# Kernel tuning notes

Measured on AMD Instinct MI355X. Metric: run time of the kernel, lower is better.

Reference implementation:

```python
import jax, jax.numpy as jnp
import numpy as np

N_NODES = 50000


def setup_inputs() -> dict:
    key = jax.random.key(0)
    k1, k2, k3, k4 = jax.random.split(key, 4)
    in_dim, out_dim, n_edges = 128, 64, 800000
    x = jax.random.normal(k1, (N_NODES, in_dim), dtype=jnp.float32)
    edge_index = jax.random.randint(k2, (2, n_edges), 0, N_NODES, dtype=jnp.int64)
    W = jax.random.normal(k3, (in_dim, out_dim), dtype=jnp.float32) * (1.0 / np.sqrt(in_dim))
    att = jax.random.normal(k4, (2 * out_dim,), dtype=jnp.float32) * (1.0 / np.sqrt(2 * out_dim))
    return {"x": x, "edge_index": edge_index, "W": W, "att": att}


def reference(x, edge_index, W, att):
    N = x.shape[0]
    F_out = W.shape[1]
    h = x @ W                                   # [N, F]
    src, dst = edge_index[0], edge_index[1]
    hs = h[src]                                 # [E, F] gather
    hd = h[dst]                                 # [E, F] gather
    # att(cat([h_src, h_dst])) == h_src @ a1 + h_dst @ a2
    a1, a2 = att[:F_out], att[F_out:]
    logit = jax.nn.leaky_relu(hs @ a1 + hd @ a2, 0.2)   # [E]
    E = logit.shape[0]
    # The original builds a dense [N, E] matrix (row d holds logit_e at col e
    # for dst[e]==d, zeros elsewhere) and softmaxes over the E axis. The
    # equivalent sparse form: denom_d = sum_{e:dst=d} exp(logit_e) + (E - deg_d)*exp(0),
    # stabilized with m_d = max(max logit over segment, 0).
    seg_max = jax.ops.segment_max(logit, dst, num_segments=N)      # -inf on empty
    m = jnp.maximum(seg_max, 0.0)                                  # include the zero cells
    exp_l = jnp.exp(logit - m[dst])                                # [E]
    seg_sum = jax.ops.segment_sum(exp_l, dst, num_segments=N)      # [N]
    deg = jax.ops.segment_sum(jnp.ones_like(logit), dst, num_segments=N)
    denom = seg_sum + (jnp.float32(E) - deg) * jnp.exp(-m)         # zeros' contribution
    w = exp_l / denom[dst]                                          # [E]
    agg = jax.ops.segment_sum(w[:, None] * hs, dst, num_segments=N)  # [N, F]
    return jax.nn.elu(agg)
```

## Files before the change

kernel.cpp:

```cpp
#include <hip/hip_runtime.h>
#include <hip/hip_bf16.h>

#define FIN 128
#define FOUT 64
#define BINW 128
#define NBINPAD 512
#define QS 2560
#define TILE 4096
#define DPQ 32
#define RCAP 768

typedef __attribute__((ext_vector_type(8))) short short8;
typedef __attribute__((ext_vector_type(4))) float f32x4;
typedef __attribute__((ext_vector_type(8))) _Float16 h8;

__device__ __forceinline__ unsigned short f2bf(float f) {
    unsigned u = __float_as_uint(f);
    unsigned r = u + 0x7FFFu + ((u >> 16) & 1u);
    return (unsigned short)(r >> 16);
}

__global__ __launch_bounds__(256) void k_prep(
    const float* __restrict__ W, const float* __restrict__ att,
    unsigned short* __restrict__ Whig, unsigned short* __restrict__ Wlog,
    float* __restrict__ wag, int* __restrict__ qcur, int nzero)
{
    const int t = threadIdx.x;
    if (blockIdx.x >= 65) {
        const int i = (blockIdx.x - 65) * 256 + t;
        if (i < nzero) qcur[i] = 0;
        return;
    }
    if (blockIdx.x == 64) {
        const int k = t & 127, which = t >> 7;
        const float* av = att + which * 64;
        const float* wr = W + k * 64;
        float acc = 0.f;
        #pragma unroll 16
        for (int n = 0; n < 64; ++n) acc += wr[n] * av[n];
        wag[which * 128 + k] = acc;
        return;
    }
    const int f = blockIdx.x * 256 + t;
    const int combo = f >> 9;
    const int s = combo >> 2, c = combo & 3;
    const int r = f & 511;
    const int l = r >> 3, j = r & 7;
    const int k = s * 32 + (l >> 4) * 8 + j;
    const int n = c * 16 + (l & 15);
    const float w = W[k * 64 + n];
    const unsigned short hi = f2bf(w);
    const float hif = __uint_as_float((unsigned)hi << 16);
    Whig[f] = hi;
    Wlog[f] = f2bf(w - hif);
}

__global__ __launch_bounds__(256) void k_fused(
    const float* __restrict__ x, const unsigned short* __restrict__ Whig,
    const unsigned short* __restrict__ Wlog, const float* __restrict__ wag,
    _Float16* __restrict__ h, float* __restrict__ as_, float* __restrict__ ad_,
    const int* __restrict__ src, const int* __restrict__ dst,
    unsigned* __restrict__ queue, int* __restrict__ qcur,
    int N, int E, int nbins, int paBlocks)
{
    union SMem {
        struct { unsigned rec[TILE]; int hist[NBINPAD]; int scanb[NBINPAD];
                 int excl[NBINPAD]; int gb[NBINPAD]; } pa;
    };
    __shared__ SMem sm;
    const int t = threadIdx.x;

    if ((int)blockIdx.x < paBlocks) {
        const int e0 = blockIdx.x * TILE;
        const int tot = (E - e0 < TILE) ? (E - e0) : TILE;
        sm.pa.hist[t] = 0; sm.pa.hist[t + 256] = 0;
        __syncthreads();
        #pragma unroll
        for (int i = 0; i < TILE / 256; ++i) {
            const int e = e0 + i * 256 + t;
            if (e < E) atomicAdd(&sm.pa.hist[__builtin_nontemporal_load(dst + e) >> 7], 1);
        }
        __syncthreads();
        const int v0 = sm.pa.hist[t], v1 = sm.pa.hist[t + 256];
        sm.pa.scanb[t] = v0; sm.pa.scanb[t + 256] = v1;
        __syncthreads();
        #pragma unroll
        for (int off = 1; off < NBINPAD; off <<= 1) {
            const int a0 = (t >= off) ? sm.pa.scanb[t - off] : 0;
            const int a1 = (t + 256 >= off) ? sm.pa.scanb[t + 256 - off] : 0;
            __syncthreads();
            sm.pa.scanb[t] += a0; sm.pa.scanb[t + 256] += a1;
            __syncthreads();
        }
        const int ex0 = sm.pa.scanb[t] - v0;
        const int ex1 = sm.pa.scanb[t + 256] - v1;
        int g0 = 0, g1 = 0;
        if (t < nbins && v0 > 0)       g0 = t * QS + atomicAdd(qcur + t, v0);
        if (t + 256 < nbins && v1 > 0) g1 = (t + 256) * QS + atomicAdd(qcur + t + 256, v1);
        sm.pa.hist[t] = ex0; sm.pa.hist[t + 256] = ex1;
        sm.pa.excl[t] = ex0; sm.pa.excl[t + 256] = ex1;
        sm.pa.gb[t] = g0;   sm.pa.gb[t + 256] = g1;
        __syncthreads();
        #pragma unroll
        for (int i = 0; i < TILE / 256; ++i) {
            const int e = e0 + i * 256 + t;
            if (e < E) {
                const int d = __builtin_nontemporal_load(dst + e);
                const int s = __builtin_nontemporal_load(src + e);
                const int pos = atomicAdd(&sm.pa.hist[d >> 7], 1);
                sm.pa.rec[pos] = (unsigned)s | ((unsigned)d << 16);
            }
        }
        __syncthreads();
        for (int i = t; i < tot; i += 256) {
            const unsigned r = sm.pa.rec[i];
            const int b = (int)(r >> 23);
            const int gpos = sm.pa.gb[b] + (i - sm.pa.excl[b]);
            if (gpos < (b + 1) * QS) queue[gpos] = r;
        }
        return;
    }

    const int bb = blockIdx.x - paBlocks;
    const int wv = t >> 6, lane = t & 63;
    const int quad = lane >> 4, mrow = lane & 15;
    const int r0 = (bb * 4 + wv) * 16;
    const int arow = r0 + mrow;
    const bool rok = arow < N;

    f32x4 acc[4] = {};
    float s1 = 0.f, s2 = 0.f;

    #pragma unroll
    for (int s = 0; s < 4; ++s) {
        float xv[8];
        if (rok) {
            const float4* p = (const float4*)(x + (size_t)arow * FIN + s * 32 + quad * 8);
            const float4 u0 = p[0], u1 = p[1];
            xv[0] = u0.x; xv[1] = u0.y; xv[2] = u0.z; xv[3] = u0.w;
            xv[4] = u1.x; xv[5] = u1.y; xv[6] = u1.z; xv[7] = u1.w;
        } else {
            #pragma unroll
            for (int j = 0; j < 8; ++j) xv[j] = 0.f;
        }
        const float4 wa0 = *(const float4*)&wag[s * 32 + quad * 8];
        const float4 wa1 = *(const float4*)&wag[s * 32 + quad * 8 + 4];
        const float4 wb0 = *(const float4*)&wag[128 + s * 32 + quad * 8];
        const float4 wb1 = *(const float4*)&wag[128 + s * 32 + quad * 8 + 4];
        const float wva[8] = {wa0.x, wa0.y, wa0.z, wa0.w, wa1.x, wa1.y, wa1.z, wa1.w};
        const float wvb[8] = {wb0.x, wb0.y, wb0.z, wb0.w, wb1.x, wb1.y, wb1.z, wb1.w};

        short8 ah, al;
        #pragma unroll
        for (int j = 0; j < 8; ++j) {
            s1 += xv[j] * wva[j];
            s2 += xv[j] * wvb[j];
            const unsigned short hi = f2bf(xv[j]);
            const float hif = __uint_as_float((unsigned)hi << 16);
            ah[j] = (short)hi;
            al[j] = (short)f2bf(xv[j] - hif);
        }
        #pragma unroll
        for (int c = 0; c < 4; ++c) {
            const short8 bh = *(const short8*)&Whig[((s * 4 + c) * 64 + lane) * 8];
            const short8 bl = *(const short8*)&Wlog[((s * 4 + c) * 64 + lane) * 8];
            acc[c] = __builtin_amdgcn_mfma_f32_16x16x32_bf16(ah, bh, acc[c], 0, 0, 0);
            acc[c] = __builtin_amdgcn_mfma_f32_16x16x32_bf16(al, bh, acc[c], 0, 0, 0);
            acc[c] = __builtin_amdgcn_mfma_f32_16x16x32_bf16(ah, bl, acc[c], 0, 0, 0);
        }
    }

    s1 += __shfl_xor(s1, 16); s1 += __shfl_xor(s1, 32);
    s2 += __shfl_xor(s2, 16); s2 += __shfl_xor(s2, 32);
    if (lane < 16 && r0 + lane < N) {
        as_[r0 + lane] = s1;
        ad_[r0 + lane] = s2;
    }

    #pragma unroll
    for (int reg = 0; reg < 4; ++reg) {
        const int orow = r0 + quad * 4 + reg;
        if (orow < N) {
            #pragma unroll
            for (int c = 0; c < 4; ++c)
                h[(size_t)orow * FOUT + c * 16 + mrow] = (_Float16)acc[c][reg];
        }
    }
}

__global__ __launch_bounds__(256) void k_aggq(
    const int* __restrict__ qcur, const unsigned* __restrict__ queue,
    const float* __restrict__ as_, const float* __restrict__ ad_,
    const _Float16* __restrict__ h, float* __restrict__ out,
    int N, float Ef)
{
    __shared__ unsigned rec[RCAP];
    __shared__ unsigned pay[RCAP];
    __shared__ int hist[DPQ], base[DPQ], cur[DPQ];
    __shared__ float adl[DPQ];
    __shared__ int nloc;

    const int bin = blockIdx.x >> 2, q = blockIdx.x & 3;
    const int d0 = bin * BINW + q * DPQ;
    const int t = threadIdx.x;
    const int wv = t >> 6, lane = t & 63;

    if (t < DPQ) {
        hist[t] = 0;
        const int d = d0 + t;
        adl[t] = (d < N) ? ad_[d] : 0.f;
    }
    if (t == 0) nloc = 0;
    __syncthreads();

    int cnt = qcur[bin];
    if (cnt > QS) cnt = QS;

    for (int i = t; i < cnt; i += 256) {
        const unsigned r = __builtin_nontemporal_load(queue + (size_t)bin * QS + i);
        if ((int)((r >> 21) & 3) == q) {
            const int p = atomicAdd(&nloc, 1);
            if (p < RCAP) rec[p] = r;
        }
    }
    __syncthreads();
    int n = nloc; if (n > RCAP) n = RCAP;

    for (int i = t; i < n; i += 256) atomicAdd(&hist[(rec[i] >> 16) & (DPQ - 1)], 1);
    __syncthreads();

    if (t < DPQ) base[t] = hist[t];
    __syncthreads();
    #pragma unroll
    for (int off = 1; off < DPQ; off <<= 1) {
        const int a = (t < DPQ && t >= off) ? base[t - off] : 0;
        __syncthreads();
        if (t < DPQ) base[t] += a;
        __syncthreads();
    }
    if (t < DPQ) { base[t] -= hist[t]; cur[t] = base[t]; }
    __syncthreads();

    for (int i = t; i < n; i += 256) {
        const unsigned r = rec[i];
        const int s  = (int)(r & 0xFFFFu);
        const int dl = (int)(r >> 16) & (DPQ - 1);
        const float z = as_[s] + adl[dl];
        const float lg = (z >= 0.f) ? z : 0.2f * z;
        const int pos = atomicAdd(&cur[dl], 1);
        pay[pos] = (unsigned)s |
            ((unsigned)__builtin_bit_cast(unsigned short, (_Float16)lg) << 16);
    }
    __syncthreads();

    const int e8 = lane >> 3, ch = lane & 7;
    for (int dl = wv; dl < DPQ; dl += 4) {
        const int d = d0 + dl;
        if (d >= N) continue;
        const int dg = hist[dl];
        const int bs = base[dl];

        float mx = -INFINITY;
        for (int j = lane; j < dg; j += 64)
            mx = fmaxf(mx, (float)__builtin_bit_cast(_Float16,
                          (unsigned short)(pay[bs + j] >> 16)));
        #pragma unroll
        for (int off = 32; off > 0; off >>= 1) mx = fmaxf(mx, __shfl_xor(mx, off));
        const float m = fmaxf(mx, 0.f);

        float ss = 0.f;
        for (int j = lane; j < dg; j += 64)
            ss += expf((float)__builtin_bit_cast(_Float16,
                       (unsigned short)(pay[bs + j] >> 16)) - m);
        #pragma unroll
        for (int off = 32; off > 0; off >>= 1) ss += __shfl_xor(ss, off);
        const float inv = 1.f / (ss + (Ef - (float)dg) * expf(-m));

        float acc[8];
        #pragma unroll
        for (int k = 0; k < 8; ++k) acc[k] = 0.f;

        for (int jb = 0; jb < dg; jb += 16) {
            const int j0 = jb + e8, j1 = jb + 8 + e8;
            float w0 = 0.f, w1 = 0.f; int s0 = 0, s1 = 0;
            if (j0 < dg) {
                const unsigned p = pay[bs + j0];
                s0 = (int)(p & 0xFFFFu);
                w0 = expf((float)__builtin_bit_cast(_Float16,
                          (unsigned short)(p >> 16)) - m) * inv;
            }
            if (j1 < dg) {
                const unsigned p = pay[bs + j1];
                s1 = (int)(p & 0xFFFFu);
                w1 = expf((float)__builtin_bit_cast(_Float16,
                          (unsigned short)(p >> 16)) - m) * inv;
            }
            const h8 hv0 = *(const h8*)(h + (size_t)s0 * FOUT + ch * 8);
            const h8 hv1 = *(const h8*)(h + (size_t)s1 * FOUT + ch * 8);
            #pragma unroll
            for (int k = 0; k < 8; ++k)
                acc[k] += w0 * (float)hv0[k] + w1 * (float)hv1[k];
        }

        #pragma unroll
        for (int k = 0; k < 8; ++k) {
            acc[k] += __shfl_xor(acc[k], 8);
            acc[k] += __shfl_xor(acc[k], 16);
            acc[k] += __shfl_xor(acc[k], 32);
        }
        if (lane < 8) {
            float r[8];
            #pragma unroll
            for (int k = 0; k < 8; ++k) r[k] = (acc[k] > 0.f) ? acc[k] : expm1f(acc[k]);
            float4* op = (float4*)(out + (size_t)d * FOUT + lane * 8);
            op[0] = make_float4(r[0], r[1], r[2], r[3]);
            op[1] = make_float4(r[4], r[5], r[6], r[7]);
        }
    }
}

extern "C" void kernel_launch(void* const* d_in, const int* in_sizes, int n_in,
                              void* d_out, int out_size, void* d_ws, size_t ws_size,
                              hipStream_t stream) {
    const float* x   = (const float*)d_in[0];
    const int*   ei  = (const int*)d_in[1];
    const float* W   = (const float*)d_in[2];
    const float* att = (const float*)d_in[3];

    const int N = in_sizes[0] / FIN;
    const int E = in_sizes[1] / 2;
    const int* src = ei;
    const int* dst = ei + E;

    const int NBINS = (N + BINW - 1) / BINW;

    char* ws = (char*)d_ws;
    size_t o = 0;
    auto carve = [&](size_t bytes) {
        void* p = ws + o; o += (bytes + 1023) & ~(size_t)1023; return p;
    };
    unsigned short* Whig = (unsigned short*)carve(16384 * 2);
    unsigned short* Wlog = (unsigned short*)carve(16384 * 2);
    float*          wag  = (float*)carve(256 * 4);
    float*          as_  = (float*)carve((size_t)N * 4);
    float*          ad_  = (float*)carve((size_t)N * 4);
    int*            qcur = (int*)carve((size_t)NBINS * 4);
    _Float16*       h    = (_Float16*)carve((size_t)N * FOUT * 2);
    unsigned*       queue = (unsigned*)carve((size_t)NBINS * QS * 4);

    float* out = (float*)d_out;

    const int paBlocks = (E + TILE - 1) / TILE;
    const int mmBlocks = (N + 63) / 64;
    const int zBlks    = (NBINS + 255) / 256;

    k_prep<<<65 + zBlks, 256, 0, stream>>>(W, att, Whig, Wlog, wag, qcur, NBINS);
    k_fused<<<paBlocks + mmBlocks, 256, 0, stream>>>(
        x, Whig, Wlog, wag, h, as_, ad_, src, dst, queue, qcur, N, E, NBINS, paBlocks);
    k_aggq<<<NBINS * 4, 256, 0, stream>>>(qcur, queue, as_, ad_, h, out, N, (float)E);
}
```

Measured before the change: 152.0 us.

## Use finer 32-node destination bins so aggregation blocks read only their own edges

The edge partitioning now buckets by dst>>5 into up to 2048 bins instead of 512 coarse bins. Each aggregation block therefore owns one 32-node bin directly, rather than four blocks rescanning and filtering the same 128-node queue. The bin-offset scan becomes a per-thread 8-element serial scan followed by a 256-wide scan. The global base offset and local exclusive offset are folded into one table. The aggregation kernel also caches the exp weights in shared memory so they are not recomputed in the weighted-sum loop. In exchange, each partition tile issues many more global atomics on the per-bin counters, and the per-bin capacity of 768 edges could overflow on skewed degree distributions.

```diff
diff --git a/kernel.cpp b/kernel.cpp
--- a/kernel.cpp
+++ b/kernel.cpp
@@ -3,12 +3,11 @@
 
 #define FIN 128
 #define FOUT 64
-#define BINW 128
-#define NBINPAD 512
-#define QS 2560
+#define BINW 32
+#define NBPAD 2048
+#define QS 768
 #define TILE 4096
-#define DPQ 32
-#define RCAP 768
+#define DPB 32
 
 typedef __attribute__((ext_vector_type(8))) short short8;
 typedef __attribute__((ext_vector_type(4))) float f32x4;
@@ -64,8 +63,7 @@
     int N, int E, int nbins, int paBlocks)
 {
     union SMem {
-        struct { unsigned rec[TILE]; int hist[NBINPAD]; int scanb[NBINPAD];
-                 int excl[NBINPAD]; int gb[NBINPAD]; } pa;
+        struct { unsigned rec[TILE]; int hist[NBPAD]; int comb[NBPAD]; int part[256]; } pa;
     };
     __shared__ SMem sm;
     const int t = threadIdx.x;
@@ -73,33 +71,39 @@
     if ((int)blockIdx.x < paBlocks) {
         const int e0 = blockIdx.x * TILE;
         const int tot = (E - e0 < TILE) ? (E - e0) : TILE;
-        sm.pa.hist[t] = 0; sm.pa.hist[t + 256] = 0;
+        for (int i = t; i < NBPAD; i += 256) sm.pa.hist[i] = 0;
         __syncthreads();
         #pragma unroll
         for (int i = 0; i < TILE / 256; ++i) {
             const int e = e0 + i * 256 + t;
-            if (e < E) atomicAdd(&sm.pa.hist[__builtin_nontemporal_load(dst + e) >> 7], 1);
-        }
-        __syncthreads();
-        const int v0 = sm.pa.hist[t], v1 = sm.pa.hist[t + 256];
-        sm.pa.scanb[t] = v0; sm.pa.scanb[t + 256] = v1;
-        __syncthreads();
-        #pragma unroll
-        for (int off = 1; off < NBINPAD; off <<= 1) {
-            const int a0 = (t >= off) ? sm.pa.scanb[t - off] : 0;
-            const int a1 = (t + 256 >= off) ? sm.pa.scanb[t + 256 - off] : 0;
+            if (e < E) atomicAdd(&sm.pa.hist[__builtin_nontemporal_load(dst + e) >> 5], 1);
+        }
+        __syncthreads();
+        int v[8], lp[8];
+        const int b0 = t * 8;
+        int run = 0;
+        #pragma unroll
+        for (int j = 0; j < 8; ++j) { v[j] = sm.pa.hist[b0 + j]; lp[j] = run; run += v[j]; }
+        sm.pa.part[t] = run;
+        __syncthreads();
+        #pragma unroll
+        for (int off = 1; off < 256; off <<= 1) {
+            const int a = (t >= off) ? sm.pa.part[t - off] : 0;
             __syncthreads();
-            sm.pa.scanb[t] += a0; sm.pa.scanb[t + 256] += a1;
+            sm.pa.part[t] += a;
             __syncthreads();
         }
-        const int ex0 = sm.pa.scanb[t] - v0;
-        const int ex1 = sm.pa.scanb[t + 256] - v1;
-        int g0 = 0, g1 = 0;
-        if (t < nbins && v0 > 0)       g0 = t * QS + atomicAdd(qcur + t, v0);
-        if (t + 256 < nbins && v1 > 0) g1 = (t + 256) * QS + atomicAdd(qcur + t + 256, v1);
-        sm.pa.hist[t] = ex0; sm.pa.hist[t + 256] = ex1;
-        sm.pa.excl[t] = ex0; sm.pa.excl[t + 256] = ex1;
-        sm.pa.gb[t] = g0;   sm.pa.gb[t + 256] = g1;
+        const int tbase = sm.pa.part[t] - run;
+        #pragma unroll
+        for (int j = 0; j < 8; ++j) {
+            const int i = b0 + j;
+            const int ex = tbase + lp[j];
+            int c = 0;
+            if (i < nbins && v[j] > 0)
+                c = i * QS + atomicAdd(qcur + i, v[j]) - ex;
+            sm.pa.comb[i] = c;
+            sm.pa.hist[i] = ex;
+        }
         __syncthreads();
         #pragma unroll
         for (int i = 0; i < TILE / 256; ++i) {
@@ -107,15 +111,15 @@
             if (e < E) {
                 const int d = __builtin_nontemporal_load(dst + e);
                 const int s = __builtin_nontemporal_load(src + e);
-                const int pos = atomicAdd(&sm.pa.hist[d >> 7], 1);
+                const int pos = atomicAdd(&sm.pa.hist[d >> 5], 1);
                 sm.pa.rec[pos] = (unsigned)s | ((unsigned)d << 16);
             }
         }
         __syncthreads();
         for (int i = t; i < tot; i += 256) {
             const unsigned r = sm.pa.rec[i];
-            const int b = (int)(r >> 23);
-            const int gpos = sm.pa.gb[b] + (i - sm.pa.excl[b]);
+            const int b = (int)(r >> 21);
+            const int gpos = sm.pa.comb[b] + i;
             if (gpos < (b + 1) * QS) queue[gpos] = r;
         }
         return;
@@ -194,23 +198,22 @@
     const _Float16* __restrict__ h, float* __restrict__ out,
     int N, float Ef)
 {
-    __shared__ unsigned rec[RCAP];
-    __shared__ unsigned pay[RCAP];
-    __shared__ int hist[DPQ], base[DPQ], cur[DPQ];
-    __shared__ float adl[DPQ];
-    __shared__ int nloc;
-
-    const int bin = blockIdx.x >> 2, q = blockIdx.x & 3;
-    const int d0 = bin * BINW + q * DPQ;
+    __shared__ unsigned rec[QS];
+    __shared__ unsigned pay[QS];
+    __shared__ float wexp[QS];
+    __shared__ int hist[DPB], base[DPB], cur[DPB];
+    __shared__ float adl[DPB];
+
+    const int bin = blockIdx.x;
+    const int d0 = bin * BINW;
     const int t = threadIdx.x;
     const int wv = t >> 6, lane = t & 63;
 
-    if (t < DPQ) {
+    if (t < DPB) {
         hist[t] = 0;
         const int d = d0 + t;
         adl[t] = (d < N) ? ad_[d] : 0.f;
     }
-    if (t == 0) nloc = 0;
     __syncthreads();
 
     int cnt = qcur[bin];
@@ -218,33 +221,27 @@
 
     for (int i = t; i < cnt; i += 256) {
         const unsigned r = __builtin_nontemporal_load(queue + (size_t)bin * QS + i);
-        if ((int)((r >> 21) & 3) == q) {
-            const int p = atomicAdd(&nloc, 1);
-            if (p < RCAP) rec[p] = r;
-        }
-    }
-    __syncthreads();
-    int n = nloc; if (n > RCAP) n = RCAP;
-
-    for (int i = t; i < n; i += 256) atomicAdd(&hist[(rec[i] >> 16) & (DPQ - 1)], 1);
-    __syncthreads();
-
-    if (t < DPQ) base[t] = hist[t];
+        rec[i] = r;
+        atomicAdd(&hist[(r >> 16) & (DPB - 1)], 1);
+    }
+    __syncthreads();
+
+    if (t < DPB) base[t] = hist[t];
     __syncthreads();
     #pragma unroll
-    for (int off = 1; off < DPQ; off <<= 1) {
-        const int a = (t < DPQ && t >= off) ? base[t - off] : 0;
-        __syncthreads();
-        if (t < DPQ) base[t] += a;
-        __syncthreads();
-    }
-    if (t < DPQ) { base[t] -= hist[t]; cur[t] = base[t]; }
-    __syncthreads();
-
-    for (int i = t; i < n; i += 256) {
+    for (int off = 1; off < DPB; off <<= 1) {
+        const int a = (t < DPB && t >= off) ? base[t - off] : 0;
+        __syncthreads();
+        if (t < DPB) base[t] += a;
+        __syncthreads();
+    }
+    if (t < DPB) { base[t] -= hist[t]; cur[t] = base[t]; }
+    __syncthreads();
+
+    for (int i = t; i < cnt; i += 256) {
         const unsigned r = rec[i];
         const int s  = (int)(r & 0xFFFFu);
-        const int dl = (int)(r >> 16) & (DPQ - 1);
+        const int dl = (int)(r >> 16) & (DPB - 1);
         const float z = as_[s] + adl[dl];
         const float lg = (z >= 0.f) ? z : 0.2f * z;
         const int pos = atomicAdd(&cur[dl], 1);
@@ -254,7 +251,7 @@
     __syncthreads();
 
     const int e8 = lane >> 3, ch = lane & 7;
-    for (int dl = wv; dl < DPQ; dl += 4) {
+    for (int dl = wv; dl < DPB; dl += 4) {
         const int d = d0 + dl;
         if (d >= N) continue;
         const int dg = hist[dl];
@@ -269,9 +266,12 @@
         const float m = fmaxf(mx, 0.f);
 
         float ss = 0.f;
-        for (int j = lane; j < dg; j += 64)
-            ss += expf((float)__builtin_bit_cast(_Float16,
+        for (int j = lane; j < dg; j += 64) {
+            const float e = expf((float)__builtin_bit_cast(_Float16,
                        (unsigned short)(pay[bs + j] >> 16)) - m);
+            wexp[bs + j] = e;
+            ss += e;
+        }
         #pragma unroll
         for (int off = 32; off > 0; off >>= 1) ss += __shfl_xor(ss, off);
         const float inv = 1.f / (ss + (Ef - (float)dg) * expf(-m));
@@ -284,16 +284,12 @@
             const int j0 = jb + e8, j1 = jb + 8 + e8;
             float w0 = 0.f, w1 = 0.f; int s0 = 0, s1 = 0;
             if (j0 < dg) {
-                const unsigned p = pay[bs + j0];
-                s0 = (int)(p & 0xFFFFu);
-                w0 = expf((float)__builtin_bit_cast(_Float16,
-                          (unsigned short)(p >> 16)) - m) * inv;
+                s0 = (int)(pay[bs + j0] & 0xFFFFu);
+                w0 = wexp[bs + j0] * inv;
             }
             if (j1 < dg) {
-                const unsigned p = pay[bs + j1];
-                s1 = (int)(p & 0xFFFFu);
-                w1 = expf((float)__builtin_bit_cast(_Float16,
-                          (unsigned short)(p >> 16)) - m) * inv;
+                s1 = (int)(pay[bs + j1] & 0xFFFFu);
+                w1 = wexp[bs + j1] * inv;
             }
             const h8 hv0 = *(const h8*)(h + (size_t)s0 * FOUT + ch * 8);
             const h8 hv1 = *(const h8*)(h + (size_t)s1 * FOUT + ch * 8);
@@ -357,5 +353,5 @@
     k_prep<<<65 + zBlks, 256, 0, stream>>>(W, att, Whig, Wlog, wag, qcur, NBINS);
     k_fused<<<paBlocks + mmBlocks, 256, 0, stream>>>(
         x, Whig, Wlog, wag, h, as_, ad_, src, dst, queue, qcur, N, E, NBINS, paBlocks);
-    k_aggq<<<NBINS * 4, 256, 0, stream>>>(qcur, queue, as_, ad_, h, out, N, (float)E);
-}
+    k_aggq<<<NBINS, 256, 0, stream>>>(qcur, queue, as_, ad_, h, out, N, (float)E);
+}
```

Measured after the change: 172.6 us. 1.14x slower.
